# Kernel tuning notes

Hardware: AMD Instinct MI355X
Metric: run time of the kernel (lower is better)

## Reference

```python
import jax, jax.numpy as jnp
import numpy as np

B, C_IN, N = 8, 32, 400000


def setup_inputs() -> dict:
    key = jax.random.key(0)
    ks = jax.random.split(key, 7)
    X = jax.random.normal(ks[0], (B, C_IN, N), dtype=jnp.float32)
    # 1x1 Conv1d weights == per-point linear layers: [out_ch, in_ch] + bias [out_ch]
    W1 = jax.random.normal(ks[1], (16, 32), dtype=jnp.float32) * (1.0 / np.sqrt(32))
    b1 = jax.random.normal(ks[2], (16,), dtype=jnp.float32) * 0.01
    W2 = jax.random.normal(ks[3], (8, 16), dtype=jnp.float32) * (1.0 / np.sqrt(16))
    b2 = jax.random.normal(ks[4], (8,), dtype=jnp.float32) * 0.01
    W3 = jax.random.normal(ks[5], (1, 8), dtype=jnp.float32) * (1.0 / np.sqrt(8))
    b3 = jax.random.normal(ks[6], (1,), dtype=jnp.float32) * 0.01
    return {"X": X, "K": 64, "W1": W1, "b1": b1, "W2": W2, "b2": b2, "W3": W3, "b3": b3}


def reference(X, K, W1, b1, W2, b2, W3, b3):
    # fc1: 1x1 conv (32->16) + ReLU
    h = jax.nn.relu(jnp.einsum('oc,bcn->bon', W1, X) + b1[None, :, None])
    # fc2: 1x1 conv (16->8) + ReLU
    h = jax.nn.relu(jnp.einsum('oc,bcn->bon', W2, h) + b2[None, :, None])
    # fc3: 1x1 conv (8->1) + Softplus -> scores [B, 1, N]
    s = jax.nn.softplus(jnp.einsum('oc,bcn->bon', W3, h) + b3[None, :, None])
    # top-K along last dim (largest, sorted -- matches torch.topk defaults)
    _, idx = jax.lax.top_k(s, K)  # [B, 1, K]
    return idx.reshape(-1)
```

## Files before the change

### kernel.cpp

```cpp
#include <hip/hip_runtime.h>
#include <math.h>

#define NPTS 400000
#define NBATCH 8
#define K_OUT 64
#define IDX_SENTINEL 0x7fffffff

#define PPW 768
#define WPB_X 131
#define LPB (WPB_X * 4)

#define WB_W2 512
#define WB_B1 640
#define WB_B2 656
#define WB_W3 664
#define WB_B3 672

__device__ __forceinline__ bool better(float av, int ai, float bv, int bi) {
    return (av > bv) || (av == bv && ai < bi);
}

__device__ __forceinline__ void cmp_swap(float& v, int& i, int j, bool keepBetter) {
    float ov = __shfl_xor(v, j);
    int   oi = __shfl_xor(i, j);
    bool ob = better(ov, oi, v, i);
    if (keepBetter ? ob : !ob) { v = ov; i = oi; }
}

__device__ __forceinline__ void wave_topk_insert(float& bv, int& bi, float nv, int ni, int lane) {
    float tv = __shfl(bv, 63);
    int   ti = __shfl(bi, 63);
    if (__ballot(better(nv, ni, tv, ti)) == 0ULL) return;
#pragma unroll
    for (int k = 2; k <= 64; k <<= 1) {
#pragma unroll
        for (int j = k >> 1; j > 0; j >>= 1) {
            bool keepBetter = (((lane & k) == 0) == ((lane & j) == 0));
            cmp_swap(nv, ni, j, keepBetter);
        }
    }
    float rv = __shfl(nv, lane ^ 63);
    int   ri = __shfl(ni, lane ^ 63);
    if (better(rv, ri, bv, bi)) { bv = rv; bi = ri; }
#pragma unroll
    for (int j = 32; j > 0; j >>= 1) cmp_swap(bv, bi, j, (lane & j) == 0);
}

__global__ __launch_bounds__(256) void prep_weights(
    const float* __restrict__ W1, const float* __restrict__ b1,
    const float* __restrict__ W2, const float* __restrict__ b2,
    const float* __restrict__ W3, const float* __restrict__ b3,
    float* __restrict__ wbuf)
{
    int t = threadIdx.x;
    for (int i = t; i < 512; i += 256) wbuf[i] = W1[(i & 15) * 32 + (i >> 4)];
    if (t < 128) wbuf[WB_W2 + t] = W2[(t & 7) * 16 + (t >> 3)];
    if (t < 16)       wbuf[WB_B1 + t] = b1[t];
    else if (t < 24)  wbuf[WB_B2 + (t - 16)] = b2[t - 16];
    else if (t < 32)  wbuf[WB_W3 + (t - 24)] = W3[t - 24];
    else if (t == 32) wbuf[WB_B3] = b3[0];
}

__device__ __forceinline__ void load_grp(const float* p, int cbase, float4 x[4]) {
#pragma unroll
    for (int j = 0; j < 4; ++j)
        x[j] = *reinterpret_cast<const float4*>(p + (size_t)(cbase + j) * NPTS);
}

__device__ __forceinline__ void fma_grp(const float* __restrict__ wb, int cbase,
                                        const float4 x[4], float4 a1[16]) {
#pragma unroll
    for (int j = 0; j < 4; ++j) {
        float4 xv = x[j];
#pragma unroll
        for (int o = 0; o < 16; ++o) {
            float w = wb[(cbase + j) * 16 + o];
            a1[o].x = fmaf(w, xv.x, a1[o].x);
            a1[o].y = fmaf(w, xv.y, a1[o].y);
            a1[o].z = fmaf(w, xv.z, a1[o].z);
            a1[o].w = fmaf(w, xv.w, a1[o].w);
        }
    }
}

__global__ __launch_bounds__(256, 4) void mlp_topk_fused(
    const float* __restrict__ X, const float* __restrict__ wb,
    int2* __restrict__ cand)
{
    int t = threadIdx.x;
    int b = blockIdx.y;
    int wave = blockIdx.x * 4 + (t >> 6);
    int lane = t & 63;
    const float* Xb = X + (size_t)b * 32 * NPTS;

    float bv = -INFINITY;
    int   bi = IDX_SENTINEL;
    int waveStart = wave * PPW;

#pragma unroll 1
    for (int it = 0; it < PPW / 256; ++it) {
        int nb = waveStart + it * 256;
        if (nb >= NPTS) break;
        int n = nb + lane * 4;
        float z0 = -INFINITY, z1 = -INFINITY, z2 = -INFINITY, z3 = -INFINITY;
        bool valid = (n < NPTS);
        if (valid) {
            const float* p = Xb + n;
            float4 xA[4], xB[4];
            float4 a1[16];
#pragma unroll
            for (int o = 0; o < 16; ++o) a1[o] = make_float4(0.f, 0.f, 0.f, 0.f);

            load_grp(p, 0, xA);
            load_grp(p, 4, xB);
            fma_grp(wb, 0, xA, a1);  load_grp(p, 8, xA);
            fma_grp(wb, 4, xB, a1);  load_grp(p, 12, xB);
            fma_grp(wb, 8, xA, a1);  load_grp(p, 16, xA);
            fma_grp(wb, 12, xB, a1); load_grp(p, 20, xB);
            fma_grp(wb, 16, xA, a1); load_grp(p, 24, xA);
            fma_grp(wb, 20, xB, a1); load_grp(p, 28, xB);
            fma_grp(wb, 24, xA, a1);
            fma_grp(wb, 28, xB, a1);

            float4 a2[8];
#pragma unroll
            for (int o = 0; o < 8; ++o) a2[o] = make_float4(0.f, 0.f, 0.f, 0.f);
#pragma unroll
            for (int c = 0; c < 16; ++c) {
                float bb = wb[WB_B1 + c];
                float4 h = a1[c];
                h.x = fmaxf(h.x + bb, 0.f);
                h.y = fmaxf(h.y + bb, 0.f);
                h.z = fmaxf(h.z + bb, 0.f);
                h.w = fmaxf(h.w + bb, 0.f);
#pragma unroll
                for (int o = 0; o < 8; ++o) {
                    float w = wb[WB_W2 + c * 8 + o];
                    a2[o].x = fmaf(w, h.x, a2[o].x);
                    a2[o].y = fmaf(w, h.y, a2[o].y);
                    a2[o].z = fmaf(w, h.z, a2[o].z);
                    a2[o].w = fmaf(w, h.w, a2[o].w);
                }
            }
            float4 zacc = make_float4(0.f, 0.f, 0.f, 0.f);
#pragma unroll
            for (int c = 0; c < 8; ++c) {
                float bb = wb[WB_B2 + c];
                float4 h = a2[c];
                h.x = fmaxf(h.x + bb, 0.f);
                h.y = fmaxf(h.y + bb, 0.f);
                h.z = fmaxf(h.z + bb, 0.f);
                h.w = fmaxf(h.w + bb, 0.f);
                float w = wb[WB_W3 + c];
                zacc.x = fmaf(w, h.x, zacc.x);
                zacc.y = fmaf(w, h.y, zacc.y);
                zacc.z = fmaf(w, h.z, zacc.z);
                zacc.w = fmaf(w, h.w, zacc.w);
            }
            float b3v = wb[WB_B3];
            z0 = zacc.x + b3v; z1 = zacc.y + b3v; z2 = zacc.z + b3v; z3 = zacc.w + b3v;
        }
        int i0 = valid ? (n + 0) : IDX_SENTINEL;
        int i1 = valid ? (n + 1) : IDX_SENTINEL;
        int i2 = valid ? (n + 2) : IDX_SENTINEL;
        int i3 = valid ? (n + 3) : IDX_SENTINEL;
        float m = fmaxf(fmaxf(z0, z1), fmaxf(z2, z3));
        float tv = __shfl(bv, 63);
        int   ti = __shfl(bi, 63);
        if (__ballot(better(m, i0, tv, ti)) == 0ULL) continue;
        wave_topk_insert(bv, bi, z0, i0, lane);
        wave_topk_insert(bv, bi, z1, i1, lane);
        wave_topk_insert(bv, bi, z2, i2, lane);
        wave_topk_insert(bv, bi, z3, i3, lane);
    }

    cand[((size_t)b * LPB + wave) * 64 + lane] = make_int2(__float_as_int(bv), bi);
}

__global__ __launch_bounds__(256) void topk_merge_k2a(
    const int2* __restrict__ cand, int2* __restrict__ cand2)
{
    __shared__ int2 sbuf[4 * 64];
    int b = blockIdx.y;
    int bk = blockIdx.x;
    int t = threadIdx.x;
    int w = t >> 6, lane = t & 63;
    const int2* cb = cand + (size_t)b * LPB * 64;

    float bv = -INFINITY;
    int   bi = IDX_SENTINEL;
    int slot = bk * 4 + w;
#pragma unroll 1
    for (int L = slot; L < LPB; L += 64) {
        int2 p = cb[(size_t)L * 64 + lane];
        wave_topk_insert(bv, bi, __int_as_float(p.x), p.y, lane);
    }
    sbuf[w * 64 + lane] = make_int2(__float_as_int(bv), bi);
    __syncthreads();

    if (w == 0) {
#pragma unroll 1
        for (int q = 1; q < 4; ++q) {
            int2 p = sbuf[q * 64 + lane];
            wave_topk_insert(bv, bi, __int_as_float(p.x), p.y, lane);
        }
        cand2[((size_t)b * 16 + bk) * 64 + lane] = make_int2(__float_as_int(bv), bi);
    }
}

__global__ __launch_bounds__(256) void topk_merge_k2b(
    const int2* __restrict__ cand2, int* __restrict__ out)
{
    __shared__ int2 sbuf[4 * 64];
    int b = blockIdx.x;
    int t = threadIdx.x;
    int w = t >> 6, lane = t & 63;
    const int2* cb = cand2 + (size_t)b * 16 * 64;

    int2 p0 = cb[(size_t)(w * 4) * 64 + lane];
    float bv = __int_as_float(p0.x);
    int   bi = p0.y;
#pragma unroll 1
    for (int q = 1; q < 4; ++q) {
        int2 p = cb[(size_t)(w * 4 + q) * 64 + lane];
        wave_topk_insert(bv, bi, __int_as_float(p.x), p.y, lane);
    }
    sbuf[w * 64 + lane] = make_int2(__float_as_int(bv), bi);
    __syncthreads();

    if (w == 0) {
#pragma unroll 1
        for (int q = 1; q < 4; ++q) {
            int2 p = sbuf[q * 64 + lane];
            wave_topk_insert(bv, bi, __int_as_float(p.x), p.y, lane);
        }
        out[b * K_OUT + lane] = bi;
    }
}

extern "C" void kernel_launch(void* const* d_in, const int* in_sizes, int n_in,
                              void* d_out, int out_size, void* d_ws, size_t ws_size,
                              hipStream_t stream) {
    const float* X  = (const float*)d_in[0];
    const float* W1 = (const float*)d_in[2];
    const float* b1 = (const float*)d_in[3];
    const float* W2 = (const float*)d_in[4];
    const float* b2 = (const float*)d_in[5];
    const float* W3 = (const float*)d_in[6];
    const float* b3 = (const float*)d_in[7];

    float* wbuf  = (float*)d_ws;
    int2*  cand  = (int2*)((char*)d_ws + 4096);
    int2*  cand2 = cand + (size_t)NBATCH * LPB * 64;
    int*   out   = (int*)d_out;

    prep_weights<<<1, 256, 0, stream>>>(W1, b1, W2, b2, W3, b3, wbuf);
    mlp_topk_fused<<<dim3(WPB_X, NBATCH), 256, 0, stream>>>(X, wbuf, cand);
    topk_merge_k2a<<<dim3(16, NBATCH), 256, 0, stream>>>(cand, cand2);
    topk_merge_k2b<<<dim3(NBATCH), 256, 0, stream>>>(cand2, out);
}
```

Before: 173.2 us.

## Stage X tiles into LDS via async global_load_lds double buffering

Replaces per-thread register-staged global float4 loads with asynchronous global-to-LDS loads (global_load_lds) into a double-buffered shared tile of 8 channels by 1024 points. Each block processes two tiles in four channel-group phases, prefetching the next phase while computing the current one, with explicit vmcnt waits and barriers. The goal is to hide HBM latency and reduce VGPR pressure so more memory can be in flight. In exchange it adds two block barriers per phase, 64KB of LDS per block (which limits occupancy), and changes the grid to 196 blocks per batch with per-wave candidate lists.

```diff
diff --git a/kernel.cpp b/kernel.cpp
--- a/kernel.cpp
+++ b/kernel.cpp
@@ -6,8 +6,10 @@
 #define K_OUT 64
 #define IDX_SENTINEL 0x7fffffff
 
-#define PPW 768
-#define WPB_X 131
+#define TILE 1024
+#define TILES_PER_BLOCK 2
+#define PPB (TILE * TILES_PER_BLOCK)
+#define WPB_X 196
 #define LPB (WPB_X * 4)
 
 #define WB_W2 512
@@ -61,67 +63,81 @@
     else if (t == 32) wbuf[WB_B3] = b3[0];
 }
 
-__device__ __forceinline__ void load_grp(const float* p, int cbase, float4 x[4]) {
-#pragma unroll
-    for (int j = 0; j < 4; ++j)
-        x[j] = *reinterpret_cast<const float4*>(p + (size_t)(cbase + j) * NPTS);
-}
-
-__device__ __forceinline__ void fma_grp(const float* __restrict__ wb, int cbase,
-                                        const float4 x[4], float4 a1[16]) {
-#pragma unroll
-    for (int j = 0; j < 4; ++j) {
-        float4 xv = x[j];
-#pragma unroll
-        for (int o = 0; o < 16; ++o) {
-            float w = wb[(cbase + j) * 16 + o];
-            a1[o].x = fmaf(w, xv.x, a1[o].x);
-            a1[o].y = fmaf(w, xv.y, a1[o].y);
-            a1[o].z = fmaf(w, xv.z, a1[o].z);
-            a1[o].w = fmaf(w, xv.w, a1[o].w);
-        }
-    }
-}
-
-__global__ __launch_bounds__(256, 4) void mlp_topk_fused(
+__device__ __forceinline__ void gld_lds16(const float* g, float* l) {
+    __builtin_amdgcn_global_load_lds(
+        (const __attribute__((address_space(1))) void*)g,
+        (__attribute__((address_space(3))) void*)l, 16, 0, 0);
+}
+
+__global__ __launch_bounds__(256) void mlp_topk_fused(
     const float* __restrict__ X, const float* __restrict__ wb,
     int2* __restrict__ cand)
 {
+    __shared__ float lds[2][8][TILE];
+
     int t = threadIdx.x;
     int b = blockIdx.y;
-    int wave = blockIdx.x * 4 + (t >> 6);
-    int lane = t & 63;
+    int wave = t >> 6, lane = t & 63;
     const float* Xb = X + (size_t)b * 32 * NPTS;
+    int bs = blockIdx.x * PPB;
+
+    int npts_blk = NPTS - bs;
+    int ntiles = (npts_blk >= PPB) ? TILES_PER_BLOCK : ((npts_blk + TILE - 1) / TILE);
+    int nph = ntiles * 4;
 
     float bv = -INFINITY;
     int   bi = IDX_SENTINEL;
-    int waveStart = wave * PPW;
-
-#pragma unroll 1
-    for (int it = 0; it < PPW / 256; ++it) {
-        int nb = waveStart + it * 256;
-        if (nb >= NPTS) break;
-        int n = nb + lane * 4;
-        float z0 = -INFINITY, z1 = -INFINITY, z2 = -INFINITY, z3 = -INFINITY;
-        bool valid = (n < NPTS);
-        if (valid) {
-            const float* p = Xb + n;
-            float4 xA[4], xB[4];
-            float4 a1[16];
+
+#define STAGE(p)                                                          \
+    {                                                                     \
+        int tile_ = (p) >> 2, cg_ = (p) & 3;                              \
+        int n4_ = bs + tile_ * TILE + t * 4;                              \
+        int off_ = (n4_ <= NPTS - 4) ? n4_ : (NPTS - 4);                  \
+        const float* src_ = Xb + off_ + (size_t)(cg_ * 8) * NPTS;         \
+        float* dst_ = &lds[(p) & 1][0][t * 4];                            \
+        _Pragma("unroll")                                                 \
+        for (int c_ = 0; c_ < 8; ++c_)                                    \
+            gld_lds16(src_ + (size_t)c_ * NPTS, dst_ + c_ * TILE);        \
+    }
+
+    float4 a1[16];
+
+    STAGE(0);
+#pragma unroll 1
+    for (int p = 0; p < nph; ++p) {
+        if (p + 1 < nph) {
+            STAGE(p + 1);
+            asm volatile("s_waitcnt vmcnt(8)" ::: "memory");
+        } else {
+            asm volatile("s_waitcnt vmcnt(0)" ::: "memory");
+        }
+        __builtin_amdgcn_s_barrier();
+
+        int tile = p >> 2, cg = p & 3;
+        if (cg == 0) {
 #pragma unroll
             for (int o = 0; o < 16; ++o) a1[o] = make_float4(0.f, 0.f, 0.f, 0.f);
-
-            load_grp(p, 0, xA);
-            load_grp(p, 4, xB);
-            fma_grp(wb, 0, xA, a1);  load_grp(p, 8, xA);
-            fma_grp(wb, 4, xB, a1);  load_grp(p, 12, xB);
-            fma_grp(wb, 8, xA, a1);  load_grp(p, 16, xA);
-            fma_grp(wb, 12, xB, a1); load_grp(p, 20, xB);
-            fma_grp(wb, 16, xA, a1); load_grp(p, 24, xA);
-            fma_grp(wb, 20, xB, a1); load_grp(p, 28, xB);
-            fma_grp(wb, 24, xA, a1);
-            fma_grp(wb, 28, xB, a1);
-
+        }
+
+        const float* lp = &lds[p & 1][0][t * 4];
+        float4 xv[8];
+#pragma unroll
+        for (int c = 0; c < 8; ++c) xv[c] = *reinterpret_cast<const float4*>(lp + c * TILE);
+#pragma unroll
+        for (int c = 0; c < 8; ++c) {
+            int ch = cg * 8 + c;
+            float4 x = xv[c];
+#pragma unroll
+            for (int o = 0; o < 16; ++o) {
+                float w = wb[ch * 16 + o];
+                a1[o].x = fmaf(w, x.x, a1[o].x);
+                a1[o].y = fmaf(w, x.y, a1[o].y);
+                a1[o].z = fmaf(w, x.z, a1[o].z);
+                a1[o].w = fmaf(w, x.w, a1[o].w);
+            }
+        }
+
+        if (cg == 3) {
             float4 a2[8];
 #pragma unroll
             for (int o = 0; o < 8; ++o) a2[o] = make_float4(0.f, 0.f, 0.f, 0.f);
@@ -158,23 +174,33 @@
                 zacc.w = fmaf(w, h.w, zacc.w);
             }
             float b3v = wb[WB_B3];
-            z0 = zacc.x + b3v; z1 = zacc.y + b3v; z2 = zacc.z + b3v; z3 = zacc.w + b3v;
-        }
-        int i0 = valid ? (n + 0) : IDX_SENTINEL;
-        int i1 = valid ? (n + 1) : IDX_SENTINEL;
-        int i2 = valid ? (n + 2) : IDX_SENTINEL;
-        int i3 = valid ? (n + 3) : IDX_SENTINEL;
-        float m = fmaxf(fmaxf(z0, z1), fmaxf(z2, z3));
-        float tv = __shfl(bv, 63);
-        int   ti = __shfl(bi, 63);
-        if (__ballot(better(m, i0, tv, ti)) == 0ULL) continue;
-        wave_topk_insert(bv, bi, z0, i0, lane);
-        wave_topk_insert(bv, bi, z1, i1, lane);
-        wave_topk_insert(bv, bi, z2, i2, lane);
-        wave_topk_insert(bv, bi, z3, i3, lane);
-    }
-
-    cand[((size_t)b * LPB + wave) * 64 + lane] = make_int2(__float_as_int(bv), bi);
+            int n = bs + tile * TILE + t * 4;
+            bool valid = (n < NPTS);
+            float z0 = valid ? zacc.x + b3v : -INFINITY;
+            float z1 = valid ? zacc.y + b3v : -INFINITY;
+            float z2 = valid ? zacc.z + b3v : -INFINITY;
+            float z3 = valid ? zacc.w + b3v : -INFINITY;
+            int i0 = valid ? (n + 0) : IDX_SENTINEL;
+            int i1 = valid ? (n + 1) : IDX_SENTINEL;
+            int i2 = valid ? (n + 2) : IDX_SENTINEL;
+            int i3 = valid ? (n + 3) : IDX_SENTINEL;
+            float m = fmaxf(fmaxf(z0, z1), fmaxf(z2, z3));
+            float tv = __shfl(bv, 63);
+            int   ti = __shfl(bi, 63);
+            if (__ballot(better(m, i0, tv, ti)) != 0ULL) {
+                wave_topk_insert(bv, bi, z0, i0, lane);
+                wave_topk_insert(bv, bi, z1, i1, lane);
+                wave_topk_insert(bv, bi, z2, i2, lane);
+                wave_topk_insert(bv, bi, z3, i3, lane);
+            }
+        }
+
+        asm volatile("s_waitcnt lgkmcnt(0)" ::: "memory");
+        __builtin_amdgcn_s_barrier();
+    }
+
+    cand[((size_t)b * LPB + blockIdx.x * 4 + wave) * 64 + lane] =
+        make_int2(__float_as_int(bv), bi);
 }
 
 __global__ __launch_bounds__(256) void topk_merge_k2a(
```

After: 224.2 us. 1.29x slower.
